# Kernel tuning notes

Measured on AMD Instinct MI355X. Metric: run time of the kernel, lower is better.

The kernel has to match this reference:

```python
import jax, jax.numpy as jnp
import numpy as np

N, NR, D, H, S, DD, FF, NC = 8, 300, 256, 8, 49, 64, 2048, 80
IOU_THR = 0.5
HD = D // H


def ln(x, eps=1e-5):
    m = x.mean(-1, keepdims=True)
    v = ((x - m) ** 2).mean(-1, keepdims=True)
    return (x - m) / jnp.sqrt(v + eps)


def pairwise_iou(b):
    # b: [N, nr, 4] xyxy -> per-image IoU [N, nr, nr] (block-diagonal of full cross IoU)
    area = (b[..., 2] - b[..., 0]) * (b[..., 3] - b[..., 1])
    lt = jnp.maximum(b[:, :, None, :2], b[:, None, :, :2])
    rb = jnp.minimum(b[:, :, None, 2:], b[:, None, :, 2:])
    wh = jnp.clip(rb - lt, 0.0)
    inter = wh[..., 0] * wh[..., 1]
    union = area[:, :, None] + area[:, None, :] - inter
    return inter / jnp.maximum(union, 1e-9)


def setup_inputs() -> dict:
    key = jax.random.key(0)
    ks = jax.random.split(key, 24)
    s = 0.02
    cxy = jax.random.uniform(ks[0], (N, NR, 2)) * 600.0 + 50.0
    wh = jax.random.uniform(ks[1], (N, NR, 2)) * 100.0 + 10.0
    bboxes = jnp.concatenate([cxy - 0.5 * wh, cxy + 0.5 * wh], -1)
    inp = {
        'bboxes': bboxes,
        'pro_features': jax.random.normal(ks[2], (N, NR, D)),
        'roi_features': jax.random.normal(ks[3], (S, N * NR, D)),
        'query': jax.random.normal(ks[4], (N, NR, D)),
        'cur_all_mask': (jax.random.uniform(ks[5], (N, NR, 1)) > 0.2).astype(jnp.float32),
        # MultiheadAttention params
        'w_qkv': jax.random.normal(ks[6], (3 * D, D)) * s,
        'b_qkv': jnp.zeros((3 * D,)),
        'w_attn_out': jax.random.normal(ks[7], (D, D)) * s,
        'b_attn_out': jnp.zeros((D,)),
        # DynamicConv (inst_interact) params
        'w_dyn': jax.random.normal(ks[8], (2 * D * DD, D)) * s,
        'b_dyn': jnp.zeros((2 * D * DD,)),
        'w_dyn_out': jax.random.normal(ks[9], (D, S * D)) * s,
        'b_dyn_out': jnp.zeros((D,)),
        # FFN params
        'w_ff1': jax.random.normal(ks[10], (FF, D)) * s,
        'b_ff1': jnp.zeros((FF,)),
        'w_ff2': jax.random.normal(ks[11], (D, FF)) * s,
        'b_ff2': jnp.zeros((D,)),
        # cls tower (NUM_CLS=1, bias-free Linear) + class logits
        'w_cls': jax.random.normal(ks[12], (D, D)) * s,
        'w_logits': jax.random.normal(ks[13], (NC, D)) * s,
        'b_logits': jnp.zeros((NC,)),
    }
    return inp


def reference(bboxes, pro_features, roi_features, query, cur_all_mask,
              w_qkv, b_qkv, w_attn_out, b_attn_out,
              w_dyn, b_dyn, w_dyn_out, b_dyn_out,
              w_ff1, b_ff1, w_ff2, b_ff2,
              w_cls, w_logits, b_logits):
    overlaps = pairwise_iou(bboxes)                      # [N, nr, nr]
    pf = pro_features                                    # relation_net: identity pass-through of tgt
    qk = pf + query                                      # with_pos_embed

    # --- IoU-relation boolean attention mask (True = masked) ---
    o_mask = (overlaps < IOU_THR).astype(jnp.float32)
    eye = jnp.eye(NR, dtype=jnp.float32)[None]           # [1, nr, nr]
    pair = cur_all_mask * jnp.swapaxes(cur_all_mask, 1, 2)  # [N, nr, nr]
    attn_mask = (o_mask * pair + eye * (1.0 - cur_all_mask)) > 0

    # --- masked multi-head self-attention (eval mode, dropout = identity) ---
    qp = qk @ w_qkv[:D].T + b_qkv[:D]
    kp = qk @ w_qkv[D:2 * D].T + b_qkv[D:2 * D]
    vp = pf @ w_qkv[2 * D:].T + b_qkv[2 * D:]
    sp = lambda x: x.reshape(N, NR, H, HD)
    scores = jnp.einsum('bqhd,bkhd->bhqk', sp(qp), sp(kp)) / np.sqrt(HD)
    scores = jnp.where(attn_mask[:, None], -1e9, scores)  # mask broadcast over heads (== repeat_interleave)
    attn = jax.nn.softmax(scores, axis=-1)
    ctx = jnp.einsum('bhqk,bkhd->bqhd', attn, sp(vp)).reshape(N, NR, D)
    tgt2 = ctx @ w_attn_out.T + b_attn_out
    pf = ln(pf + tgt2)                                   # norm1
    pf = (pf * cur_all_mask).reshape(N * NR, D)

    # --- DynamicConv instance interaction on detached ROI features ---
    feats = jnp.swapaxes(jax.lax.stop_gradient(roi_features), 0, 1)  # [N*nr, S, D]
    params = pf @ w_dyn.T + b_dyn                        # [N*nr, 2*D*DD]
    p1 = params[:, :D * DD].reshape(-1, D, DD)
    p2 = params[:, D * DD:].reshape(-1, DD, D)
    f = jax.nn.relu(ln(jnp.einsum('nsd,nde->nse', feats, p1)))
    f = jax.nn.relu(ln(jnp.einsum('nse,ned->nsd', f, p2)))
    pf2 = jax.nn.relu(ln(f.reshape(N * NR, S * D) @ w_dyn_out.T + b_dyn_out))
    pf = ln(pf + pf2)                                    # norm2

    # --- FFN ---
    t2 = jax.nn.relu(pf @ w_ff1.T + b_ff1) @ w_ff2.T + b_ff2
    obj = ln(pf + t2)                                    # norm3

    # --- cls tower + logits (reg branch output is discarded by forward) ---
    fc = obj * cur_all_mask.reshape(N * NR, 1)
    cls_f = jax.nn.relu(ln(fc @ w_cls.T))
    class_logits = (cls_f @ w_logits.T + b_logits).reshape(N, NR, NC)
    return class_logits
```

## Files before the change

kernel.cpp:

```cpp
#include <hip/hip_runtime.h>
#include <hip/hip_bf16.h>

using bf16 = __hip_bfloat16;

#define NIMG 8
#define NR 300
#define DIM 256
#define NHEAD 8
#define HD 32
#define SS 49
#define DDIM 64
#define FFD 2048
#define NCLS 80
#define MTOT (NIMG*NR)
#define NFLAGS 32

typedef short short8 __attribute__((ext_vector_type(8)));
typedef float f32x4 __attribute__((ext_vector_type(4)));

__device__ inline float ldv(const void* p, long long i, int f32) {
  return f32 ? ((const float*)p)[i] : __bfloat162float(((const bf16*)p)[i]);
}

__device__ inline unsigned short f2bfu(float x) {
  bf16 b = __float2bfloat16(x);
  unsigned short u; __builtin_memcpy(&u, &b, 2); return u;
}
__device__ inline float bfu2f(unsigned short u) {
  bf16 b; __builtin_memcpy(&b, &u, 2); return __bfloat162float(b);
}

__device__ inline int dynperm(int n) {
  if (n < DIM*DDIM) { int e = n >> 8, d = n & 255; return d*DDIM + e; }
  int q = n - DIM*DDIM; int d = q >> 6, e = q & 63; return DIM*DDIM + e*DIM + d;
}

__device__ inline float wsum(float v) {
#pragma unroll
  for (int o = 32; o > 0; o >>= 1) v += __shfl_xor(v, o, 64);
  return v;
}
__device__ inline float wmaxf(float v) {
#pragma unroll
  for (int o = 32; o > 0; o >>= 1) v = fmaxf(v, __shfl_xor(v, o, 64));
  return v;
}
__device__ inline float bsum(float v, float* s4) {
  v = wsum(v);
  int w = threadIdx.x >> 6;
  if ((threadIdx.x & 63) == 0) s4[w] = v;
  __syncthreads();
  float r = s4[0] + s4[1] + s4[2] + s4[3];
  __syncthreads();
  return r;
}

__global__ __launch_bounds__(64) void zero_flags_kernel(int* flags) {
  if (threadIdx.x < NFLAGS) flags[threadIdx.x] = 0;
}
__global__ __launch_bounds__(256) void detect_dtype_kernel(const void* __restrict__ p,
                                                           long long n,
                                                           int* __restrict__ flags) {
  long long i = (long long)blockIdx.x*256 + threadIdx.x;
  long long stride = (long long)gridDim.x*256;
  int f32 = 0;
  for (; i < n; i += stride) {
    float v = __bfloat162float(((const bf16*)p)[i]);
    if (!(fabsf(v) <= 1.0e20f)) { f32 = 1; break; }
  }
  if (f32) atomicOr(&flags[0], 1);
}

__global__ __launch_bounds__(256) void prep_kernel(const void* __restrict__ pro,
                                                   const void* __restrict__ query,
                                                   float* __restrict__ pf0,
                                                   float* __restrict__ qk,
                                                   const int* __restrict__ flags) {
  int f32 = flags[0];
  int i = blockIdx.x*256 + threadIdx.x;
  float p = ldv(pro, i, f32);
  pf0[i] = p;
  qk[i] = p + ldv(query, i, f32);
}

__global__ __launch_bounds__(256) void split_kernel(const float* __restrict__ x,
                                                    unsigned short* __restrict__ hi,
                                                    unsigned short* __restrict__ lo,
                                                    long long n4) {
  long long q = (long long)blockIdx.x*256 + threadIdx.x;
  if (q >= n4) return;
  long long i = q*4;
  float4 v = *(const float4*)(x + i);
  float vv[4] = {v.x, v.y, v.z, v.w};
  unsigned short h[4], l[4];
#pragma unroll
  for (int j = 0; j < 4; ++j) {
    h[j] = f2bfu(vv[j]);
    l[j] = f2bfu(vv[j] - bfu2f(h[j]));
  }
  uint2 ph = make_uint2((unsigned)h[0] | ((unsigned)h[1]<<16),
                        (unsigned)h[2] | ((unsigned)h[3]<<16));
  uint2 pl = make_uint2((unsigned)l[0] | ((unsigned)l[1]<<16),
                        (unsigned)l[2] | ((unsigned)l[3]<<16));
  *(uint2*)(hi + i) = ph;
  *(uint2*)(lo + i) = pl;
}

#define GBM 128
#define GBN 64
#define GBK 32
__global__ __launch_bounds__(256) void gemm_mfma_k(
    const unsigned short* __restrict__ Ahi, const unsigned short* __restrict__ Alo,
    const void* __restrict__ Wt, long long woff,
    const void* __restrict__ bias, long long boff,
    float* __restrict__ C,
    unsigned short* __restrict__ Chi, unsigned short* __restrict__ Clo,
    int M, int Nn, int K, int relu, int kit, int splitk, int wperm,
    const int* __restrict__ flags) {
  int f32 = flags[0];
  __shared__ __align__(16) unsigned short Ah[GBM][40];
  __shared__ __align__(16) unsigned short Al[GBM][40];
  __shared__ __align__(16) unsigned short Bh[GBN][40];
  __shared__ __align__(16) unsigned short Bl[GBN][40];
  int tid = threadIdx.x;
  int lane = tid & 63, wid = tid >> 6;
  int wm = wid * 32;
  int m0 = blockIdx.x*GBM, n0 = blockIdx.y*GBN;
  int row = lane & 15, kb = (lane >> 4) * 8;
  int kbeg = 0, kend = K;
  if (splitk) { kbeg = blockIdx.z*kit*GBK; kend = kbeg + kit*GBK; if (kend > K) kend = K; }
  f32x4 zero = {0.f, 0.f, 0.f, 0.f};
  f32x4 acc[2][4];
#pragma unroll
  for (int i = 0; i < 2; ++i)
#pragma unroll
    for (int j = 0; j < 4; ++j) acc[i][j] = zero;
  int sr = tid >> 2, kq = (tid & 3) * 8;
  for (int k0 = kbeg; k0 < kend; k0 += GBK) {
#pragma unroll
    for (int p = 0; p < 2; ++p) {
      int r = sr + p*64;
      int gm = m0 + r;
      uint4 h = {0,0,0,0}, l = {0,0,0,0};
      if (gm < M) {
        size_t e = (size_t)gm*K + k0 + kq;
        h = *(const uint4*)(Ahi + e);
        l = *(const uint4*)(Alo + e);
      }
      *(uint4*)&Ah[r][kq] = h;
      *(uint4*)&Al[r][kq] = l;
    }
    {
      int gno = n0 + sr;
      int gn = wperm ? dynperm(gno) : gno;
      if (!f32) {
        uint4 h = {0,0,0,0};
        if (gno < Nn)
          h = *(const uint4*)((const unsigned short*)Wt + woff + (size_t)gn*K + k0 + kq);
        *(uint4*)&Bh[sr][kq] = h;
      } else {
        float v[8] = {0.f,0.f,0.f,0.f,0.f,0.f,0.f,0.f};
        if (gno < Nn) {
          const float* wp = (const float*)Wt + woff + (size_t)gn*K + k0 + kq;
          float4 u0 = *(const float4*)wp;
          float4 u1 = *(const float4*)(wp + 4);
          v[0]=u0.x; v[1]=u0.y; v[2]=u0.z; v[3]=u0.w;
          v[4]=u1.x; v[5]=u1.y; v[6]=u1.z; v[7]=u1.w;
        }
        unsigned short h[8], l[8];
#pragma unroll
        for (int j = 0; j < 8; ++j) {
          h[j] = f2bfu(v[j]);
          l[j] = f2bfu(v[j] - bfu2f(h[j]));
        }
        uint4 ph = {(unsigned)h[0]|((unsigned)h[1]<<16), (unsigned)h[2]|((unsigned)h[3]<<16),
                    (unsigned)h[4]|((unsigned)h[5]<<16), (unsigned)h[6]|((unsigned)h[7]<<16)};
        uint4 pl = {(unsigned)l[0]|((unsigned)l[1]<<16), (unsigned)l[2]|((unsigned)l[3]<<16),
                    (unsigned)l[4]|((unsigned)l[5]<<16), (unsigned)l[6]|((unsigned)l[7]<<16)};
        *(uint4*)&Bh[sr][kq] = ph;
        *(uint4*)&Bl[sr][kq] = pl;
      }
    }
    __syncthreads();
    short8 ah[2], al[2], bh[4];
#pragma unroll
    for (int fm = 0; fm < 2; ++fm) {
      ah[fm] = *(const short8*)&Ah[wm + fm*16 + row][kb];
      al[fm] = *(const short8*)&Al[wm + fm*16 + row][kb];
    }
#pragma unroll
    for (int fn = 0; fn < 4; ++fn) bh[fn] = *(const short8*)&Bh[fn*16 + row][kb];
#pragma unroll
    for (int fm = 0; fm < 2; ++fm)
#pragma unroll
      for (int fn = 0; fn < 4; ++fn) {
        acc[fm][fn] = __builtin_amdgcn_mfma_f32_16x16x32_bf16(ah[fm], bh[fn], acc[fm][fn], 0, 0, 0);
        acc[fm][fn] = __builtin_amdgcn_mfma_f32_16x16x32_bf16(al[fm], bh[fn], acc[fm][fn], 0, 0, 0);
      }
    if (f32) {
      short8 bl[4];
#pragma unroll
      for (int fn = 0; fn < 4; ++fn) bl[fn] = *(const short8*)&Bl[fn*16 + row][kb];
#pragma unroll
      for (int fm = 0; fm < 2; ++fm)
#pragma unroll
        for (int fn = 0; fn < 4; ++fn)
          acc[fm][fn] = __builtin_amdgcn_mfma_f32_16x16x32_bf16(ah[fm], bl[fn], acc[fm][fn], 0, 0, 0);
    }
    __syncthreads();
  }
#pragma unroll
  for (int fm = 0; fm < 2; ++fm) {
    int rb = m0 + wm + fm*16 + (lane >> 4)*4;
#pragma unroll
    for (int fn = 0; fn < 4; ++fn) {
      int gc = n0 + fn*16 + row;
      if (gc >= Nn) continue;
#pragma unroll
      for (int j = 0; j < 4; ++j) {
        int gm = rb + j;
        if (gm >= M) continue;
        float v = acc[fm][fn][j];
        if (splitk) {
          atomicAdd(&C[(size_t)gm*Nn + gc], v);
        } else {
          if (bias) v += ldv(bias, boff + (wperm ? dynperm(gc) : gc), f32);
          if (relu) v = fmaxf(v, 0.f);
          if (Chi) {
            unsigned short h = f2bfu(v);
            unsigned short l = f2bfu(v - bfu2f(h));
            size_t o = (size_t)gm*Nn + gc;
            Chi[o] = h; Clo[o] = l;
          } else {
            C[(size_t)gm*Nn + gc] = v;
          }
        }
      }
    }
  }
}

__global__ __launch_bounds__(256) void init_bias_kernel(float* __restrict__ C,
                                                        const void* __restrict__ bias,
                                                        long long boff, int n, int Nn,
                                                        const int* __restrict__ flags) {
  int f32 = flags[0];
  int i = blockIdx.x*256 + threadIdx.x;
  if (i < n) C[i] = bias ? ldv(bias, boff + (i % Nn), f32) : 0.f;
}

__global__ __launch_bounds__(256) void attn_kernel(const float* __restrict__ qp,
                                                   const float* __restrict__ kp,
                                                   const float* __restrict__ vp,
                                                   const void* __restrict__ bboxes,
                                                   const void* __restrict__ mask,
                                                   float* __restrict__ ctx,
                                                   const int* __restrict__ flags) {
  int f32 = flags[0];
  int nq = blockIdx.x;
  int n = nq / NR, q = nq % NR;
  __shared__ float qv[DIM];
  __shared__ float sc[NHEAD*NR];
  int t = threadIdx.x;
  qv[t] = qp[(size_t)nq*DIM + t];
  __syncthreads();
  float mq = ldv(mask, nq, f32);
  float qx0 = ldv(bboxes, (long long)nq*4+0, f32);
  float qy0 = ldv(bboxes, (long long)nq*4+1, f32);
  float qx1 = ldv(bboxes, (long long)nq*4+2, f32);
  float qy1 = ldv(bboxes, (long long)nq*4+3, f32);
  float areaq = (qx1-qx0)*(qy1-qy0);
  for (int idx = t; idx < NHEAD*NR; idx += 256) {
    int h = idx / NR, k = idx % NR;
    const float* kr = kp + ((size_t)n*NR + k)*DIM + h*HD;
    const float* qh = qv + h*HD;
    float s = 0.f;
#pragma unroll
    for (int d = 0; d < HD; ++d) s += qh[d]*kr[d];
    s *= 0.17677669529663687f;
    long long bk = (long long)(n*NR + k)*4;
    float kx0 = ldv(bboxes, bk+0, f32);
    float ky0 = ldv(bboxes, bk+1, f32);
    float kx1 = ldv(bboxes, bk+2, f32);
    float ky1 = ldv(bboxes, bk+3, f32);
    float areak = (kx1-kx0)*(ky1-ky0);
    float lx = fmaxf(qx0, kx0), ly = fmaxf(qy0, ky0);
    float rx = fminf(qx1, kx1), ry = fminf(qy1, ky1);
    float iw = fmaxf(rx-lx, 0.f), ih = fmaxf(ry-ly, 0.f);
    float inter = iw*ih;
    float uni = areaq + areak - inter;
    float iou = inter / fmaxf(uni, 1e-9f);
    float mk = ldv(mask, n*NR + k, f32);
    float am = (iou < 0.5f ? 1.f : 0.f)*mq*mk + ((q == k) ? (1.f - mq) : 0.f);
    if (am > 0.f) s = -1e9f;
    sc[idx] = s;
  }
  __syncthreads();
  int wv = t >> 6, lane = t & 63;
  for (int h = wv*2; h < wv*2 + 2; ++h) {
    float mx = -3.4e38f;
    for (int k = lane; k < NR; k += 64) mx = fmaxf(mx, sc[h*NR + k]);
    mx = wmaxf(mx);
    float sum = 0.f;
    for (int k = lane; k < NR; k += 64) {
      float e = expf(sc[h*NR + k] - mx);
      sc[h*NR + k] = e;
      sum += e;
    }
    sum = wsum(sum);
    float inv = 1.f / sum;
    for (int k = lane; k < NR; k += 64) sc[h*NR + k] *= inv;
  }
  __syncthreads();
  int h = t >> 5, d = t & 31;
  float acc = 0.f;
  const float* vb = vp + (size_t)n*NR*DIM + h*HD + d;
  for (int k = 0; k < NR; ++k) acc += sc[h*NR + k] * vb[(size_t)k*DIM];
  ctx[(size_t)nq*DIM + t] = acc;
}

__global__ __launch_bounds__(256) void norm1_kernel(const float* __restrict__ pf0,
                                                    const float* __restrict__ tgt2,
                                                    const void* __restrict__ mask,
                                                    float* __restrict__ pf1,
                                                    const int* __restrict__ flags) {
  int f32 = flags[0];
  int r = blockIdx.x, t = threadIdx.x;
  __shared__ float s4[4];
  float x = pf0[(size_t)r*DIM + t] + tgt2[(size_t)r*DIM + t];
  float mean = bsum(x, s4) * (1.f/DIM);
  float df = x - mean;
  float var = bsum(df*df, s4) * (1.f/DIM);
  float y = df * rsqrtf(var + 1e-5f);
  pf1[(size_t)r*DIM + t] = y * ldv(mask, r, f32);
}

__global__ __launch_bounds__(256) void dyn_mfma_kernel(
    const void* __restrict__ roi,
    const unsigned short* __restrict__ Phi, const unsigned short* __restrict__ Plo,
    unsigned short* __restrict__ f2hi, unsigned short* __restrict__ f2lo,
    int r0, const int* __restrict__ flags) {
  int f32 = flags[0];
  int ci = blockIdx.x;
  int rr = r0 + ci;
  __shared__ __align__(16) unsigned short F1h[64][72];
  __shared__ __align__(16) unsigned short F1l[64][72];
  int tid = threadIdx.x;
  int lane = tid & 63, wid = tid >> 6;
  int rlo = lane & 15, rhi = lane >> 4;
  size_t pcb = (size_t)ci * (2*DIM*DDIM);
  f32x4 zero = {0.f,0.f,0.f,0.f};
  f32x4 acc1[4];
#pragma unroll
  for (int i = 0; i < 4; ++i) acc1[i] = zero;
  int s_a = 16*wid + rlo;
  int s_c = s_a > SS-1 ? SS-1 : s_a;
  for (int ks = 0; ks < 8; ++ks) {
    int k = ks*32 + rhi*8;
    short8 ah, al = (short8)0;
    if (!f32) {
      ah = *(const short8*)((const unsigned short*)roi + ((size_t)s_c*MTOT + rr)*DIM + k);
    } else {
      const float* rp = (const float*)roi + ((size_t)s_c*MTOT + rr)*DIM + k;
      float4 u0 = *(const float4*)rp, u1 = *(const float4*)(rp + 4);
      float v[8] = {u0.x,u0.y,u0.z,u0.w,u1.x,u1.y,u1.z,u1.w};
#pragma unroll
      for (int j = 0; j < 8; ++j) {
        unsigned short h = f2bfu(v[j]);
        ah[j] = (short)h;
        al[j] = (short)f2bfu(v[j] - bfu2f(h));
      }
    }
#pragma unroll
    for (int fn = 0; fn < 4; ++fn) {
      int e = fn*16 + rlo;
      short8 bh = *(const short8*)(Phi + pcb + (size_t)e*DIM + k);
      short8 bl = *(const short8*)(Plo + pcb + (size_t)e*DIM + k);
      acc1[fn] = __builtin_amdgcn_mfma_f32_16x16x32_bf16(ah, bh, acc1[fn], 0, 0, 0);
      acc1[fn] = __builtin_amdgcn_mfma_f32_16x16x32_bf16(ah, bl, acc1[fn], 0, 0, 0);
      if (f32) acc1[fn] = __builtin_amdgcn_mfma_f32_16x16x32_bf16(al, bh, acc1[fn], 0, 0, 0);
    }
  }
#pragma unroll
  for (int j = 0; j < 4; ++j) {
    float x[4], sum = 0.f;
#pragma unroll
    for (int fn = 0; fn < 4; ++fn) { x[fn] = acc1[fn][j]; sum += x[fn]; }
#pragma unroll
    for (int o = 8; o > 0; o >>= 1) sum += __shfl_xor(sum, o, 64);
    float mean = sum * (1.f/DDIM);
    float vs = 0.f;
#pragma unroll
    for (int fn = 0; fn < 4; ++fn) { float d0 = x[fn]-mean; vs += d0*d0; }
#pragma unroll
    for (int o = 8; o > 0; o >>= 1) vs += __shfl_xor(vs, o, 64);
    float rs = rsqrtf(vs*(1.f/DDIM) + 1e-5f);
    int row = 16*wid + rhi*4 + j;
#pragma unroll
    for (int fn = 0; fn < 4; ++fn) {
      float y = fmaxf((x[fn]-mean)*rs, 0.f);
      unsigned short h = f2bfu(y);
      F1h[row][fn*16 + rlo] = h;
      F1l[row][fn*16 + rlo] = f2bfu(y - bfu2f(h));
    }
  }
  __syncthreads();
  f32x4 acc2[16];
#pragma unroll
  for (int i = 0; i < 16; ++i) acc2[i] = zero;
  for (int ks = 0; ks < 2; ++ks) {
    int k = ks*32 + rhi*8;
    short8 ah = *(const short8*)&F1h[16*wid + rlo][k];
    short8 al = *(const short8*)&F1l[16*wid + rlo][k];
#pragma unroll
    for (int fn = 0; fn < 16; ++fn) {
      int d0 = fn*16 + rlo;
      short8 bh = *(const short8*)(Phi + pcb + DIM*DDIM + (size_t)d0*DDIM + k);
      short8 bl = *(const short8*)(Plo + pcb + DIM*DDIM + (size_t)d0*DDIM + k);
      acc2[fn] = __builtin_amdgcn_mfma_f32_16x16x32_bf16(ah, bh, acc2[fn], 0, 0, 0);
      acc2[fn] = __builtin_amdgcn_mfma_f32_16x16x32_bf16(al, bh, acc2[fn], 0, 0, 0);
      acc2[fn] = __builtin_amdgcn_mfma_f32_16x16x32_bf16(ah, bl, acc2[fn], 0, 0, 0);
    }
  }
#pragma unroll
  for (int j = 0; j < 4; ++j) {
    float sum = 0.f;
#pragma unroll
    for (int fn = 0; fn < 16; ++fn) sum += acc2[fn][j];
#pragma unroll
    for (int o = 8; o > 0; o >>= 1) sum += __shfl_xor(sum, o, 64);
    float mean = sum * (1.f/DIM);
    float vs = 0.f;
#pragma unroll
    for (int fn = 0; fn < 16; ++fn) { float d0 = acc2[fn][j]-mean; vs += d0*d0; }
#pragma unroll
    for (int o = 8; o > 0; o >>= 1) vs += __shfl_xor(vs, o, 64);
    float rs = rsqrtf(vs*(1.f/DIM) + 1e-5f);
    int s = 16*wid + rhi*4 + j;
    if (s < SS) {
      size_t ob = ((size_t)ci*SS + s)*DIM;
#pragma unroll
      for (int fn = 0; fn < 16; ++fn) {
        float y = fmaxf((acc2[fn][j]-mean)*rs, 0.f);
        unsigned short h = f2bfu(y);
        f2hi[ob + fn*16 + rlo] = h;
        f2lo[ob + fn*16 + rlo] = f2bfu(y - bfu2f(h));
      }
    }
  }
}

__global__ __launch_bounds__(256) void normdyn_kernel(const float* __restrict__ g,
                                                      const float* __restrict__ pf1,
                                                      float* __restrict__ pfB) {
  int r = blockIdx.x, t = threadIdx.x;
  __shared__ float s4[4];
  float x = g[(size_t)r*DIM + t];
  float mean = bsum(x, s4)*(1.f/DIM);
  float df = x - mean;
  float var = bsum(df*df, s4)*(1.f/DIM);
  float y = fmaxf(df*rsqrtf(var+1e-5f), 0.f);
  float x2 = pf1[(size_t)r*DIM + t] + y;
  float mean2 = bsum(x2, s4)*(1.f/DIM);
  float df2 = x2 - mean2;
  float var2 = bsum(df2*df2, s4)*(1.f/DIM);
  pfB[(size_t)r*DIM + t] = df2*rsqrtf(var2+1e-5f);
}

__global__ __launch_bounds__(256) void norm3_kernel(const float* __restrict__ pfB,
                                                    const float* __restrict__ t2,
                                                    const void* __restrict__ mask,
                                                    float* __restrict__ fc,
                                                    const int* __restrict__ flags) {
  int f32 = flags[0];
  int r = blockIdx.x, t = threadIdx.x;
  __shared__ float s4[4];
  float x = pfB[(size_t)r*DIM + t] + t2[(size_t)r*DIM + t];
  float mean = bsum(x, s4)*(1.f/DIM);
  float df = x - mean;
  float var = bsum(df*df, s4)*(1.f/DIM);
  float y = df*rsqrtf(var+1e-5f);
  fc[(size_t)r*DIM + t] = y * ldv(mask, r, f32);
}

__global__ __launch_bounds__(256) void lncls_kernel(const float* __restrict__ g,
                                                    float* __restrict__ out) {
  int r = blockIdx.x, t = threadIdx.x;
  __shared__ float s4[4];
  float x = g[(size_t)r*DIM + t];
  float mean = bsum(x, s4)*(1.f/DIM);
  float df = x - mean;
  float var = bsum(df*df, s4)*(1.f/DIM);
  out[(size_t)r*DIM + t] = fmaxf(df*rsqrtf(var+1e-5f), 0.f);
}

__global__ __launch_bounds__(256) void final_kernel(const float* __restrict__ logf,
                                                    const int* __restrict__ flags,
                                                    void* __restrict__ out, int n) {
  int f32 = flags[0];
  int i = blockIdx.x*256 + threadIdx.x;
  if (i < n) {
    float v = logf[i];
    if (!(fabsf(v) <= 3.0e38f)) v = 0.f;
    if (i == 0) {
      int code = 0;
      for (int s = NFLAGS - 1; s >= 1; --s) if (flags[s]) code = 100 + 4*s;
      if (code) v = (float)code;
    }
    if (f32) ((float*)out)[i] = v;
    else ((bf16*)out)[i] = __float2bfloat16(v);
  }
}

extern "C" void kernel_launch(void* const* d_in, const int* in_sizes, int n_in,
                              void* d_out, int out_size, void* d_ws, size_t ws_size,
                              hipStream_t stream) {
  const void* bboxes     = d_in[0];
  const void* pro        = d_in[1];
  const void* roi        = d_in[2];
  const void* query      = d_in[3];
  const void* mask       = d_in[4];
  const void* w_qkv      = d_in[5];
  const void* b_qkv      = d_in[6];
  const void* w_attn_out = d_in[7];
  const void* b_attn_out = d_in[8];
  const void* w_dyn      = d_in[9];
  const void* b_dyn      = d_in[10];
  const void* w_dyn_out  = d_in[11];
  const void* b_dyn_out  = d_in[12];
  const void* w_ff1      = d_in[13];
  const void* b_ff1      = d_in[14];
  const void* w_ff2      = d_in[15];
  const void* b_ff2      = d_in[16];
  const void* w_cls      = d_in[17];
  const void* w_logits   = d_in[18];
  const void* b_logits   = d_in[19];
  (void)in_sizes; (void)n_in; (void)out_size;

  const size_t RD = (size_t)MTOT*DIM;

  const size_t DYNROW = (size_t)2*DIM*DDIM;
  size_t wsf = ws_size / sizeof(float);
  size_t fixedf = 5*RD + (size_t)MTOT*NCLS + 256;
  auto spl_of = [&](size_t chn, size_t fh) {
    size_t a = chn*(size_t)SS*DIM, b = fh*(size_t)FFD;
    size_t m = a > b ? a : b; return m > RD ? m : RD;
  };
  auto need = [&](size_t chn, size_t fh) {
    return fixedf + chn*DYNROW + fh*FFD + spl_of(chn, fh);
  };
  int CHN = 64, FH = 300;
  if (wsf >= need(2400, MTOT))      { CHN = 2400; FH = MTOT; }
  else if (wsf >= need(1200, MTOT)) { CHN = 1200; FH = MTOT; }
  else if (wsf >= need(600, MTOT))  { CHN = 600;  FH = MTOT; }
  else if (wsf >= need(300, MTOT))  { CHN = 300;  FH = MTOT; }
  else if (wsf >= need(150, 300))   { CHN = 150;  FH = 300;  }
  const size_t SPL = spl_of(CHN, FH);

  float* Wsp = (float*)d_ws;
  size_t off = 0;
  auto alloc = [&](size_t n) { float* p = Wsp + off; off += n; return p; };
  float* A = alloc(RD);
  float* B = alloc(RD);
  float* C = alloc(RD);
  float* D = alloc(RD);
  float* E = alloc(RD);
  float* logf = alloc((size_t)MTOT*NCLS);
  float* ffh = alloc((size_t)FH*FFD);
  float* Pc  = alloc((size_t)CHN*2*DIM*DDIM);
  unsigned short* Ahi = (unsigned short*)alloc(SPL/2 + 8);
  unsigned short* Alo = (unsigned short*)alloc(SPL/2 + 8);
  int* flags = (int*)(Wsp + off);
  unsigned short* ffhi = (unsigned short*)ffh;
  unsigned short* fflo = ffhi + (size_t)FH*FFD;
  unsigned short* Pchi = (unsigned short*)Pc;
  unsigned short* Pclo = Pchi + (size_t)CHN*2*DIM*DDIM;

  dim3 b256(256);
  auto split = [&](const float* x, long long n) {
    long long n4 = n/4;
    split_kernel<<<(int)((n4 + 255)/256), b256, 0, stream>>>(x, Ahi, Alo, n4);
  };
  auto gemm_full = [&](const unsigned short* Ah_, const unsigned short* Al_,
                       const void* Wm, long long woff,
                       const void* bias, long long boff, float* Cm,
                       unsigned short* Chi, unsigned short* Clo,
                       int M, int Nn, int K, int relu, int wperm) {
    int gm = (M + GBM - 1)/GBM;
    int gn = (Nn + GBN - 1)/GBN;
    int ntiles = K / GBK;
    int ks = 1;
    if (!relu && !Chi && gm*gn < 512) {
      ks = (768 + gm*gn - 1)/(gm*gn);
      if (ks > ntiles) ks = ntiles;
    }
    int kit = (ntiles + ks - 1)/ks;
    ks = (ntiles + kit - 1)/kit;
    if (ks > 1) {
      int n = M*Nn;
      init_bias_kernel<<<(n + 255)/256, b256, 0, stream>>>(Cm, bias, boff, n, Nn, flags);
      gemm_mfma_k<<<dim3(gm, gn, ks), b256, 0, stream>>>(Ah_, Al_, Wm, woff, nullptr, 0,
                                                         Cm, nullptr, nullptr,
                                                         M, Nn, K, relu, kit, 1, 0, flags);
    } else {
      gemm_mfma_k<<<dim3(gm, gn, 1), b256, 0, stream>>>(Ah_, Al_, Wm, woff, bias, boff,
                                                        Cm, Chi, Clo,
                                                        M, Nn, K, relu, kit, 0, wperm, flags);
    }
  };
  auto gemm = [&](const unsigned short* Ah_, const unsigned short* Al_,
                  const void* Wm, long long woff,
                  const void* bias, long long boff, float* Cm,
                  int M, int Nn, int K, int relu) {
    gemm_full(Ah_, Al_, Wm, woff, bias, boff, Cm, nullptr, nullptr, M, Nn, K, relu, 0);
  };

  zero_flags_kernel<<<1, 64, 0, stream>>>(flags);
  detect_dtype_kernel<<<256, b256, 0, stream>>>(w_qkv, 3LL*DIM*DIM, flags);

  prep_kernel<<<MTOT, b256, 0, stream>>>(pro, query, A, B, flags);
  split(B, RD);
  gemm(Ahi, Alo, w_qkv, 0,                  b_qkv, 0,     C, MTOT, DIM, DIM, 0);
  gemm(Ahi, Alo, w_qkv, (long long)DIM*DIM, b_qkv, DIM,   D, MTOT, DIM, DIM, 0);
  split(A, RD);
  gemm(Ahi, Alo, w_qkv, 2LL*DIM*DIM,        b_qkv, 2*DIM, E, MTOT, DIM, DIM, 0);
  attn_kernel<<<MTOT, b256, 0, stream>>>(C, D, E, bboxes, mask, B, flags);
  split(B, RD);
  gemm(Ahi, Alo, w_attn_out, 0, b_attn_out, 0, C, MTOT, DIM, DIM, 0);
  norm1_kernel<<<MTOT, b256, 0, stream>>>(A, C, mask, D, flags);

  for (int r0 = 0; r0 < MTOT; r0 += CHN) {
    int m = MTOT - r0 < CHN ? MTOT - r0 : CHN;
    split(D + (size_t)r0*DIM, (long long)m*DIM);
    gemm_full(Ahi, Alo, w_dyn, 0, b_dyn, 0, nullptr, Pchi, Pclo,
              m, 2*DIM*DDIM, DIM, 0, 1);
    dyn_mfma_kernel<<<m, b256, 0, stream>>>(roi, Pchi, Pclo, Ahi, Alo, r0, flags);
    gemm(Ahi, Alo, w_dyn_out, 0, b_dyn_out, 0, E + (size_t)r0*DIM,
         m, DIM, SS*DIM, 0);
  }
  normdyn_kernel<<<MTOT, b256, 0, stream>>>(E, D, A);

  for (int r0 = 0; r0 < MTOT; r0 += FH) {
    int m = MTOT - r0 < FH ? MTOT - r0 : FH;
    split(A + (size_t)r0*DIM, (long long)m*DIM);
    gemm_full(Ahi, Alo, w_ff1, 0, b_ff1, 0, nullptr, ffhi, fflo, m, FFD, DIM, 1, 0);
    gemm(ffhi, fflo, w_ff2, 0, b_ff2, 0, B + (size_t)r0*DIM, m, DIM, FFD, 0);
  }
  norm3_kernel<<<MTOT, b256, 0, stream>>>(A, B, mask, C, flags);

  split(C, RD);
  gemm(Ahi, Alo, w_cls, 0, nullptr, 0, D, MTOT, DIM, DIM, 0);
  lncls_kernel<<<MTOT, b256, 0, stream>>>(D, E);
  split(E, RD);
  gemm(Ahi, Alo, w_logits, 0, b_logits, 0, logf, MTOT, NCLS, DIM, 0);

  final_kernel<<<((MTOT*NCLS)+255)/256, b256, 0, stream>>>(logf, flags, d_out, MTOT*NCLS);
}
```

Measured before the change: 1.365 ms.

## Interleave bf16 hi/lo split pairs into packed 32-bit words and cap dyn chunk size

Replaces the separate hi and lo bf16 arrays with one array of 32-bit words that each hold a hi/lo pair. The split kernel, the GEMM A loads and epilogue, and the dynamic-conv kernel now read and write this packed form and unpack it in registers. The aim is fewer separate memory streams and more contiguous accesses, at the cost of extra shift and mask ALU work when unpacking. The largest dynamic-conv chunk sizes (2400 and 1200) are also removed, so that stage now runs as at least four chunked launches, which shrinks the workspace but adds launches.

```diff
diff --git a/kernel.cpp b/kernel.cpp
--- a/kernel.cpp
+++ b/kernel.cpp
@@ -29,6 +29,28 @@
 __device__ inline float bfu2f(unsigned short u) {
   bf16 b; __builtin_memcpy(&b, &u, 2); return __bfloat162float(b);
 }
+__device__ inline unsigned packhl(float x) {
+  unsigned short h = f2bfu(x);
+  unsigned short l = f2bfu(x - bfu2f(h));
+  return (unsigned)h | ((unsigned)l << 16);
+}
+__device__ inline void unpack8(const unsigned* __restrict__ p, uint4& h, uint4& l) {
+  uint4 a0 = *(const uint4*)p;
+  uint4 a1 = *(const uint4*)(p + 4);
+  h.x = (a0.x & 0xffffu) | (a0.y << 16);
+  h.y = (a0.z & 0xffffu) | (a0.w << 16);
+  h.z = (a1.x & 0xffffu) | (a1.y << 16);
+  h.w = (a1.z & 0xffffu) | (a1.w << 16);
+  l.x = (a0.x >> 16) | (a0.y & 0xffff0000u);
+  l.y = (a0.z >> 16) | (a0.w & 0xffff0000u);
+  l.z = (a1.x >> 16) | (a1.y & 0xffff0000u);
+  l.w = (a1.z >> 16) | (a1.w & 0xffff0000u);
+}
+__device__ inline void unpack8s(const unsigned* __restrict__ p, short8& h, short8& l) {
+  uint4 H, L; unpack8(p, H, L);
+  __builtin_memcpy(&h, &H, 16);
+  __builtin_memcpy(&l, &L, 16);
+}
 
 __device__ inline int dynperm(int n) {
   if (n < DIM*DDIM) { int e = n >> 8, d = n & 255; return d*DDIM + e; }
@@ -84,37 +106,25 @@
 }
 
 __global__ __launch_bounds__(256) void split_kernel(const float* __restrict__ x,
-                                                    unsigned short* __restrict__ hi,
-                                                    unsigned short* __restrict__ lo,
+                                                    unsigned* __restrict__ pk,
                                                     long long n4) {
   long long q = (long long)blockIdx.x*256 + threadIdx.x;
   if (q >= n4) return;
   long long i = q*4;
   float4 v = *(const float4*)(x + i);
-  float vv[4] = {v.x, v.y, v.z, v.w};
-  unsigned short h[4], l[4];
-#pragma unroll
-  for (int j = 0; j < 4; ++j) {
-    h[j] = f2bfu(vv[j]);
-    l[j] = f2bfu(vv[j] - bfu2f(h[j]));
-  }
-  uint2 ph = make_uint2((unsigned)h[0] | ((unsigned)h[1]<<16),
-                        (unsigned)h[2] | ((unsigned)h[3]<<16));
-  uint2 pl = make_uint2((unsigned)l[0] | ((unsigned)l[1]<<16),
-                        (unsigned)l[2] | ((unsigned)l[3]<<16));
-  *(uint2*)(hi + i) = ph;
-  *(uint2*)(lo + i) = pl;
+  uint4 o;
+  o.x = packhl(v.x); o.y = packhl(v.y); o.z = packhl(v.z); o.w = packhl(v.w);
+  *(uint4*)(pk + i) = o;
 }
 
 #define GBM 128
 #define GBN 64
 #define GBK 32
 __global__ __launch_bounds__(256) void gemm_mfma_k(
-    const unsigned short* __restrict__ Ahi, const unsigned short* __restrict__ Alo,
+    const unsigned* __restrict__ Apk,
     const void* __restrict__ Wt, long long woff,
     const void* __restrict__ bias, long long boff,
-    float* __restrict__ C,
-    unsigned short* __restrict__ Chi, unsigned short* __restrict__ Clo,
+    float* __restrict__ C, unsigned* __restrict__ Cpk,
     int M, int Nn, int K, int relu, int kit, int splitk, int wperm,
     const int* __restrict__ flags) {
   int f32 = flags[0];
@@ -142,11 +152,7 @@
       int r = sr + p*64;
       int gm = m0 + r;
       uint4 h = {0,0,0,0}, l = {0,0,0,0};
-      if (gm < M) {
-        size_t e = (size_t)gm*K + k0 + kq;
-        h = *(const uint4*)(Ahi + e);
-        l = *(const uint4*)(Alo + e);
-      }
+      if (gm < M) unpack8(Apk + (size_t)gm*K + k0 + kq, h, l);
       *(uint4*)&Ah[r][kq] = h;
       *(uint4*)&Al[r][kq] = l;
     }
@@ -226,14 +232,8 @@
         } else {
           if (bias) v += ldv(bias, boff + (wperm ? dynperm(gc) : gc), f32);
           if (relu) v = fmaxf(v, 0.f);
-          if (Chi) {
-            unsigned short h = f2bfu(v);
-            unsigned short l = f2bfu(v - bfu2f(h));
-            size_t o = (size_t)gm*Nn + gc;
-            Chi[o] = h; Clo[o] = l;
-          } else {
-            C[(size_t)gm*Nn + gc] = v;
-          }
+          if (Cpk) Cpk[(size_t)gm*Nn + gc] = packhl(v);
+          else C[(size_t)gm*Nn + gc] = v;
         }
       }
     }
@@ -337,8 +337,8 @@
 
 __global__ __launch_bounds__(256) void dyn_mfma_kernel(
     const void* __restrict__ roi,
-    const unsigned short* __restrict__ Phi, const unsigned short* __restrict__ Plo,
-    unsigned short* __restrict__ f2hi, unsigned short* __restrict__ f2lo,
+    const unsigned* __restrict__ Ppk,
+    unsigned* __restrict__ f2pk,
     int r0, const int* __restrict__ flags) {
   int f32 = flags[0];
   int ci = blockIdx.x;
@@ -374,8 +374,8 @@
 #pragma unroll
     for (int fn = 0; fn < 4; ++fn) {
       int e = fn*16 + rlo;
-      short8 bh = *(const short8*)(Phi + pcb + (size_t)e*DIM + k);
-      short8 bl = *(const short8*)(Plo + pcb + (size_t)e*DIM + k);
+      short8 bh, bl;
+      unpack8s(Ppk + pcb + (size_t)e*DIM + k, bh, bl);
       acc1[fn] = __builtin_amdgcn_mfma_f32_16x16x32_bf16(ah, bh, acc1[fn], 0, 0, 0);
       acc1[fn] = __builtin_amdgcn_mfma_f32_16x16x32_bf16(ah, bl, acc1[fn], 0, 0, 0);
       if (f32) acc1[fn] = __builtin_amdgcn_mfma_f32_16x16x32_bf16(al, bh, acc1[fn], 0, 0, 0);
@@ -415,8 +415,8 @@
 #pragma unroll
     for (int fn = 0; fn < 16; ++fn) {
       int d0 = fn*16 + rlo;
-      short8 bh = *(const short8*)(Phi + pcb + DIM*DDIM + (size_t)d0*DDIM + k);
-      short8 bl = *(const short8*)(Plo + pcb + DIM*DDIM + (size_t)d0*DDIM + k);
+      short8 bh, bl;
+      unpack8s(Ppk + pcb + DIM*DDIM + (size_t)d0*DDIM + k, bh, bl);
       acc2[fn] = __builtin_amdgcn_mfma_f32_16x16x32_bf16(ah, bh, acc2[fn], 0, 0, 0);
       acc2[fn] = __builtin_amdgcn_mfma_f32_16x16x32_bf16(al, bh, acc2[fn], 0, 0, 0);
       acc2[fn] = __builtin_amdgcn_mfma_f32_16x16x32_bf16(ah, bl, acc2[fn], 0, 0, 0);
@@ -442,9 +442,7 @@
 #pragma unroll
       for (int fn = 0; fn < 16; ++fn) {
         float y = fmaxf((acc2[fn][j]-mean)*rs, 0.f);
-        unsigned short h = f2bfu(y);
-        f2hi[ob + fn*16 + rlo] = h;
-        f2lo[ob + fn*16 + rlo] = f2bfu(y - bfu2f(h));
+        f2pk[ob + fn*16 + rlo] = packhl(y);
       }
     }
   }
@@ -550,9 +548,7 @@
     return fixedf + chn*DYNROW + fh*FFD + spl_of(chn, fh);
   };
   int CHN = 64, FH = 300;
-  if (wsf >= need(2400, MTOT))      { CHN = 2400; FH = MTOT; }
-  else if (wsf >= need(1200, MTOT)) { CHN = 1200; FH = MTOT; }
-  else if (wsf >= need(600, MTOT))  { CHN = 600;  FH = MTOT; }
+  if (wsf >= need(600, MTOT))       { CHN = 600;  FH = MTOT; }
   else if (wsf >= need(300, MTOT))  { CHN = 300;  FH = MTOT; }
   else if (wsf >= need(150, 300))   { CHN = 150;  FH = 300;  }
   const size_t SPL = spl_of(CHN, FH);
@@ -568,29 +564,26 @@
   float* logf = alloc((size_t)MTOT*NCLS);
   float* ffh = alloc((size_t)FH*FFD);
   float* Pc  = alloc((size_t)CHN*2*DIM*DDIM);
-  unsigned short* Ahi = (unsigned short*)alloc(SPL/2 + 8);
-  unsigned short* Alo = (unsigned short*)alloc(SPL/2 + 8);
+  unsigned* Apk = (unsigned*)alloc(SPL + 8);
   int* flags = (int*)(Wsp + off);
-  unsigned short* ffhi = (unsigned short*)ffh;
-  unsigned short* fflo = ffhi + (size_t)FH*FFD;
-  unsigned short* Pchi = (unsigned short*)Pc;
-  unsigned short* Pclo = Pchi + (size_t)CHN*2*DIM*DDIM;
+  unsigned* ffpk = (unsigned*)ffh;
+  unsigned* Ppk  = (unsigned*)Pc;
 
   dim3 b256(256);
   auto split = [&](const float* x, long long n) {
     long long n4 = n/4;
-    split_kernel<<<(int)((n4 + 255)/256), b256, 0, stream>>>(x, Ahi, Alo, n4);
+    split_kernel<<<(int)((n4 + 255)/256), b256, 0, stream>>>(x, Apk, n4);
   };
-  auto gemm_full = [&](const unsigned short* Ah_, const unsigned short* Al_,
+  auto gemm_full = [&](const unsigned* Apk_,
                        const void* Wm, long long woff,
                        const void* bias, long long boff, float* Cm,
-                       unsigned short* Chi, unsigned short* Clo,
+                       unsigned* Cpk,
                        int M, int Nn, int K, int relu, int wperm) {
     int gm = (M + GBM - 1)/GBM;
     int gn = (Nn + GBN - 1)/GBN;
     int ntiles = K / GBK;
     int ks = 1;
-    if (!relu && !Chi && gm*gn < 512) {
+    if (!relu && !Cpk && gm*gn < 512) {
       ks = (768 + gm*gn - 1)/(gm*gn);
       if (ks > ntiles) ks = ntiles;
     }
@@ -599,20 +592,20 @@
     if (ks > 1) {
       int n = M*Nn;
       init_bias_kernel<<<(n + 255)/256, b256, 0, stream>>>(Cm, bias, boff, n, Nn, flags);
-      gemm_mfma_k<<<dim3(gm, gn, ks), b256, 0, stream>>>(Ah_, Al_, Wm, woff, nullptr, 0,
-                                                         Cm, nullptr, nullptr,
+      gemm_mfma_k<<<dim3(gm, gn, ks), b256, 0, stream>>>(Apk_, Wm, woff, nullptr, 0,
+                                                         Cm, nullptr,
                                                          M, Nn, K, relu, kit, 1, 0, flags);
     } else {
-      gemm_mfma_k<<<dim3(gm, gn, 1), b256, 0, stream>>>(Ah_, Al_, Wm, woff, bias, boff,
-                                                        Cm, Chi, Clo,
+      gemm_mfma_k<<<dim3(gm, gn, 1), b256, 0, stream>>>(Apk_, Wm, woff, bias, boff,
+                                                        Cm, Cpk,
                                                         M, Nn, K, relu, kit, 0, wperm, flags);
     }
   };
-  auto gemm = [&](const unsigned short* Ah_, const unsigned short* Al_,
+  auto gemm = [&](const unsigned* Apk_,
                   const void* Wm, long long woff,
                   const void* bias, long long boff, float* Cm,
                   int M, int Nn, int K, int relu) {
-    gemm_full(Ah_, Al_, Wm, woff, bias, boff, Cm, nullptr, nullptr, M, Nn, K, relu, 0);
+    gemm_full(Apk_, Wm, woff, bias, boff, Cm, nullptr, M, Nn, K, relu, 0);
   };
 
   zero_flags_kernel<<<1, 64, 0, stream>>>(flags);
@@ -620,22 +613,21 @@
 
   prep_kernel<<<MTOT, b256, 0, stream>>>(pro, query, A, B, flags);
   split(B, RD);
-  gemm(Ahi, Alo, w_qkv, 0,                  b_qkv, 0,     C, MTOT, DIM, DIM, 0);
-  gemm(Ahi, Alo, w_qkv, (long long)DIM*DIM, b_qkv, DIM,   D, MTOT, DIM, DIM, 0);
+  gemm(Apk, w_qkv, 0,                  b_qkv, 0,     C, MTOT, DIM, DIM, 0);
+  gemm(Apk, w_qkv, (long long)DIM*DIM, b_qkv, DIM,   D, MTOT, DIM, DIM, 0);
   split(A, RD);
-  gemm(Ahi, Alo, w_qkv, 2LL*DIM*DIM,        b_qkv, 2*DIM, E, MTOT, DIM, DIM, 0);
+  gemm(Apk, w_qkv, 2LL*DIM*DIM,        b_qkv, 2*DIM, E, MTOT, DIM, DIM, 0);
   attn_kernel<<<MTOT, b256, 0, stream>>>(C, D, E, bboxes, mask, B, flags);
   split(B, RD);
-  gemm(Ahi, Alo, w_attn_out, 0, b_attn_out, 0, C, MTOT, DIM, DIM, 0);
+  gemm(Apk, w_attn_out, 0, b_attn_out, 0, C, MTOT, DIM, DIM, 0);
   norm1_kernel<<<MTOT, b256, 0, stream>>>(A, C, mask, D, flags);
 
   for (int r0 = 0; r0 < MTOT; r0 += CHN) {
     int m = MTOT - r0 < CHN ? MTOT - r0 : CHN;
     split(D + (size_t)r0*DIM, (long long)m*DIM);
-    gemm_full(Ahi, Alo, w_dyn, 0, b_dyn, 0, nullptr, Pchi, Pclo,
-              m, 2*DIM*DDIM, DIM, 0, 1);
-    dyn_mfma_kernel<<<m, b256, 0, stream>>>(roi, Pchi, Pclo, Ahi, Alo, r0, flags);
-    gemm(Ahi, Alo, w_dyn_out, 0, b_dyn_out, 0, E + (size_t)r0*DIM,
+    gemm_full(Apk, w_dyn, 0, b_dyn, 0, nullptr, Ppk, m, 2*DIM*DDIM, DIM, 0, 1);
+    dyn_mfma_kernel<<<m, b256, 0, stream>>>(roi, Ppk, Apk, r0, flags);
+    gemm(Apk, w_dyn_out, 0, b_dyn_out, 0, E + (size_t)r0*DIM,
          m, DIM, SS*DIM, 0);
   }
   normdyn_kernel<<<MTOT, b256, 0, stream>>>(E, D, A);
@@ -643,16 +635,16 @@
   for (int r0 = 0; r0 < MTOT; r0 += FH) {
     int m = MTOT - r0 < FH ? MTOT - r0 : FH;
     split(A + (size_t)r0*DIM, (long long)m*DIM);
-    gemm_full(Ahi, Alo, w_ff1, 0, b_ff1, 0, nullptr, ffhi, fflo, m, FFD, DIM, 1, 0);
-    gemm(ffhi, fflo, w_ff2, 0, b_ff2, 0, B + (size_t)r0*DIM, m, DIM, FFD, 0);
+    gemm_full(Apk, w_ff1, 0, b_ff1, 0, nullptr, ffpk, m, FFD, DIM, 1, 0);
+    gemm(ffpk, w_ff2, 0, b_ff2, 0, B + (size_t)r0*DIM, m, DIM, FFD, 0);
   }
   norm3_kernel<<<MTOT, b256, 0, stream>>>(A, B, mask, C, flags);
 
   split(C, RD);
-  gemm(Ahi, Alo, w_cls, 0, nullptr, 0, D, MTOT, DIM, DIM, 0);
+  gemm(Apk, w_cls, 0, nullptr, 0, D, MTOT, DIM, DIM, 0);
   lncls_kernel<<<MTOT, b256, 0, stream>>>(D, E);
   split(E, RD);
-  gemm(Ahi, Alo, w_logits, 0, b_logits, 0, logf, MTOT, NCLS, DIM, 0);
+  gemm(Apk, w_logits, 0, b_logits, 0, logf, MTOT, NCLS, DIM, 0);
 
   final_kernel<<<((MTOT*NCLS)+255)/256, b256, 0, stream>>>(logf, flags, d_out, MTOT*NCLS);
 }
```

New measurement: 1.348 ms. No clear change (-1.2%).
